# Optimization experiments

Hardware: AMD Instinct MI355X
Metric: run time of the kernel (lower is better)

Reference implementation:

```python
import jax, jax.numpy as jnp
import numpy as np

N_USER = 100000
N_ITEM = 100000
E = 500000
IN, HID, OUT = 128, 128, 64
ETYPES = ["rates", "rated_by", "follows", "similar"]
# canonical etypes: (user,rates,item), (item,rated_by,user), (user,follows,user), (item,similar,item)
SRC_N = {"rates": N_USER, "rated_by": N_ITEM, "follows": N_USER, "similar": N_ITEM}
DST_N = {"rates": N_ITEM, "rated_by": N_USER, "follows": N_USER, "similar": N_ITEM}


def setup_inputs() -> dict:
    key = jax.random.key(0)
    ks = iter(jax.random.split(key, 64))
    inp = {}
    inp["emb_user"] = jax.random.normal(next(ks), (N_USER, IN), jnp.float32)
    inp["emb_item"] = jax.random.normal(next(ks), (N_ITEM, IN), jnp.float32)
    for et in ETYPES:
        inp[f"W1_{et}"] = jax.random.normal(next(ks), (IN, HID), jnp.float32) / np.float32(np.sqrt(IN))
        inp[f"b1_{et}"] = jnp.zeros((HID,), jnp.float32)
        inp[f"W2_{et}"] = jax.random.normal(next(ks), (HID, OUT), jnp.float32) / np.float32(np.sqrt(HID))
        inp[f"b2_{et}"] = jnp.zeros((OUT,), jnp.float32)
    for et in ETYPES:
        inp[f"src_{et}"] = jax.random.randint(next(ks), (E,), 0, SRC_N[et], jnp.int32)
        inp[f"dst_{et}"] = jax.random.randint(next(ks), (E,), 0, DST_N[et], jnp.int32)
    return inp


def _mean_agg(Wh, src, dst, n_dst):
    """copy_u('Wh','m') + mean('m','h') for one relation."""
    m = jnp.take(Wh, src, axis=0)                                   # [E, d] gather
    s = jax.ops.segment_sum(m, dst, num_segments=n_dst)             # [n_dst, d]
    cnt = jax.ops.segment_sum(jnp.ones(src.shape, Wh.dtype), dst, num_segments=n_dst)
    return s / jnp.maximum(cnt, 1.0)[:, None]                       # zero-indegree -> 0


def _layer(xu, xi, Wr, br, Wrb, brb, Wf, bf, Ws, bs,
           s_r, d_r, s_rb, d_rb, s_f, d_f, s_s, d_s):
    # cross-etype 'sum' reducer
    h_user = (_mean_agg(xi @ Wrb + brb, s_rb, d_rb, N_USER)
              + _mean_agg(xu @ Wf + bf, s_f, d_f, N_USER))
    h_item = (_mean_agg(xu @ Wr + br, s_r, d_r, N_ITEM)
              + _mean_agg(xi @ Ws + bs, s_s, d_s, N_ITEM))
    return h_user, h_item


def reference(emb_user, emb_item,
              W1_rates, b1_rates, W1_rated_by, b1_rated_by, W1_follows, b1_follows, W1_similar, b1_similar,
              W2_rates, b2_rates, W2_rated_by, b2_rated_by, W2_follows, b2_follows, W2_similar, b2_similar,
              src_rates, dst_rates, src_rated_by, dst_rated_by,
              src_follows, dst_follows, src_similar, dst_similar):
    hu, hi = _layer(emb_user, emb_item,
                    W1_rates, b1_rates, W1_rated_by, b1_rated_by,
                    W1_follows, b1_follows, W1_similar, b1_similar,
                    src_rates, dst_rates, src_rated_by, dst_rated_by,
                    src_follows, dst_follows, src_similar, dst_similar)
    hu = jax.nn.leaky_relu(hu)  # torch F.leaky_relu default slope 0.01
    hi = jax.nn.leaky_relu(hi)
    ou, oi = _layer(hu, hi,
                    W2_rates, b2_rates, W2_rated_by, b2_rated_by,
                    W2_follows, b2_follows, W2_similar, b2_similar,
                    src_rates, dst_rates, src_rated_by, dst_rated_by,
                    src_follows, dst_follows, src_similar, dst_similar)
    return ou  # ret_obj == 'user'
```

## Files before the change

### kernel.cpp

```cpp
#include <hip/hip_runtime.h>
#include <hip/hip_fp16.h>

#define N_USER 100000
#define N_ITEM 100000
#define NEDGE  500000
#define NKEY   400000
#define BSHIFT 11
#define NB     196
#define BCAP   11264
#define TILE   4096

#define SEG_RATES    0
#define SEG_RATED_BY 100000
#define SEG_FOLLOWS  200000
#define SEG_SIMILAR  300000

typedef _Float16 f16x8 __attribute__((ext_vector_type(8)));
typedef float    f32x4 __attribute__((ext_vector_type(4)));

__global__ void prep_w_all(const float* __restrict__ W0, const float* __restrict__ W1,
                           const float* __restrict__ W2, const float* __restrict__ W3,
                           const float* __restrict__ W4, const float* __restrict__ W5,
                           __half* __restrict__ D0, __half* __restrict__ D1,
                           __half* __restrict__ D2, __half* __restrict__ D3,
                           __half* __restrict__ D4, __half* __restrict__ D5)
{
    int y = blockIdx.y;
    const float* W = y == 0 ? W0 : y == 1 ? W1 : y == 2 ? W2 : y == 3 ? W3 : y == 4 ? W4 : W5;
    __half* dst    = y == 0 ? D0 : y == 1 ? D1 : y == 2 ? D2 : y == 3 ? D3 : y == 4 ? D4 : D5;
    int N = y < 4 ? 128 : 64;
    int i = blockIdx.x * 256 + threadIdx.x;
    if (i >= 128 * N) return;
    int k = i / N, n = i % N;
    int chunk = (n >> 4) * 4 + (k >> 5);
    int lane  = ((k >> 3) & 3) * 16 + (n & 15);
    int e     = k & 7;
    dst[(chunk * 64 + lane) * 8 + e] = __float2half(W[i]);
}

__global__ __launch_bounds__(256, 3)
void gemm2(const float* __restrict__ A,
           const __half* __restrict__ Wf0, const __half* __restrict__ Wf1,
           const float* __restrict__ b0, const float* __restrict__ b1,
           __half* __restrict__ out0, __half* __restrict__ out1, int M)
{
    const int tid = threadIdx.x;
    const int wave = tid >> 6, lane = tid & 63;
    const int l16 = lane & 15, lk = lane >> 4;
    const int rowBase = blockIdx.x * 64 + wave * 16;

    f32x4 acc0[8], acc1[8];
#pragma unroll
    for (int n = 0; n < 8; ++n) { acc0[n] = (f32x4)0.f; acc1[n] = (f32x4)0.f; }

    const int gr = rowBase + l16;
    const bool valid = gr < M;
    const float* ap = A + (size_t)(valid ? gr : 0) * 128 + lk * 8;
    float4 av[8];
#pragma unroll
    for (int kt = 0; kt < 4; ++kt) {
        av[2 * kt]     = *reinterpret_cast<const float4*>(ap + kt * 32);
        av[2 * kt + 1] = *reinterpret_cast<const float4*>(ap + kt * 32 + 4);
    }
    if (!valid) {
#pragma unroll
        for (int j = 0; j < 8; ++j) av[j] = make_float4(0.f, 0.f, 0.f, 0.f);
    }

#pragma unroll
    for (int kt = 0; kt < 4; ++kt) {
        f16x8 af;
        af[0] = (_Float16)av[2 * kt].x;     af[1] = (_Float16)av[2 * kt].y;
        af[2] = (_Float16)av[2 * kt].z;     af[3] = (_Float16)av[2 * kt].w;
        af[4] = (_Float16)av[2 * kt + 1].x; af[5] = (_Float16)av[2 * kt + 1].y;
        af[6] = (_Float16)av[2 * kt + 1].z; af[7] = (_Float16)av[2 * kt + 1].w;
#pragma unroll
        for (int n = 0; n < 8; ++n) {
            const size_t cidx = (size_t)((n * 4 + kt) * 64 + lane) * 8;
            f16x8 bf0 = *reinterpret_cast<const f16x8*>(Wf0 + cidx);
            f16x8 bf1 = *reinterpret_cast<const f16x8*>(Wf1 + cidx);
            acc0[n] = __builtin_amdgcn_mfma_f32_16x16x32_f16(af, bf0, acc0[n], 0, 0, 0);
            acc1[n] = __builtin_amdgcn_mfma_f32_16x16x32_f16(af, bf1, acc1[n], 0, 0, 0);
        }
    }

    const int gr0 = rowBase + lk * 4;
#pragma unroll
    for (int n = 0; n < 8; ++n) {
        float bv0 = b0[n * 16 + l16];
        float bv1 = b1[n * 16 + l16];
#pragma unroll
        for (int r = 0; r < 4; ++r) {
            int grr = gr0 + r;
            if (grr < M) {
                out0[(size_t)grr * 128 + n * 16 + l16] = __float2half(acc0[n][r] + bv0);
                out1[(size_t)grr * 128 + n * 16 + l16] = __float2half(acc1[n][r] + bv1);
            }
        }
    }
}

__global__ __launch_bounds__(256, 4)
void gemm1_l2_pair(const __half* __restrict__ A0, const __half* __restrict__ A1,
                   const __half* __restrict__ Wf0, const __half* __restrict__ Wf1,
                   const float* __restrict__ bias0, const float* __restrict__ bias1,
                   __half* __restrict__ O0, __half* __restrict__ O1, int M)
{
    const __half* A  = blockIdx.y ? A1 : A0;
    const __half* Wf = blockIdx.y ? Wf1 : Wf0;
    const float* bias = blockIdx.y ? bias1 : bias0;
    __half* out = blockIdx.y ? O1 : O0;

    const int tid = threadIdx.x;
    const int wave = tid >> 6, lane = tid & 63;
    const int l16 = lane & 15, lk = lane >> 4;
    const int rowBase = blockIdx.x * 128 + wave * 32;

    f32x4 acc[2][4];
#pragma unroll
    for (int m = 0; m < 2; ++m)
#pragma unroll
        for (int n = 0; n < 4; ++n) acc[m][n] = (f32x4)0.f;

#pragma unroll
    for (int kt = 0; kt < 4; ++kt) {
        f16x8 af[2];
#pragma unroll
        for (int m = 0; m < 2; ++m) {
            int gr = rowBase + m * 16 + l16;
            f16x8 a = (f16x8)(_Float16)0.f;
            if (gr < M)
                a = *reinterpret_cast<const f16x8*>(&A[(size_t)gr * 128 + kt * 32 + lk * 8]);
#pragma unroll
            for (int e = 0; e < 8; ++e) {
                float x = (float)a[e];
                x = x > 0.f ? x : 0.01f * x;
                a[e] = (_Float16)x;
            }
            af[m] = a;
        }
#pragma unroll
        for (int n = 0; n < 4; ++n) {
            const size_t cidx = (size_t)((n * 4 + kt) * 64 + lane) * 8;
            f16x8 bf = *reinterpret_cast<const f16x8*>(Wf + cidx);
            acc[0][n] = __builtin_amdgcn_mfma_f32_16x16x32_f16(af[0], bf, acc[0][n], 0, 0, 0);
            acc[1][n] = __builtin_amdgcn_mfma_f32_16x16x32_f16(af[1], bf, acc[1][n], 0, 0, 0);
        }
    }

#pragma unroll
    for (int m = 0; m < 2; ++m) {
        int gr0 = rowBase + m * 16 + lk * 4;
#pragma unroll
        for (int n = 0; n < 4; ++n) {
            float bv = bias[n * 16 + l16];
#pragma unroll
            for (int r = 0; r < 4; ++r) {
                int gr = gr0 + r;
                if (gr < M)
                    out[(size_t)gr * 64 + n * 16 + l16] = __float2half(acc[m][n][r] + bv);
            }
        }
    }
}

__global__ __launch_bounds__(256)
void partition_kernel(const int* __restrict__ s0, const int* __restrict__ d0,
                      const int* __restrict__ s1, const int* __restrict__ d1,
                      const int* __restrict__ s2, const int* __restrict__ d2,
                      const int* __restrict__ s3, const int* __restrict__ d3,
                      int* __restrict__ bucket_cursor, uint2* __restrict__ pairbuf)
{
    __shared__ int cntS[256], lscan[256], gbase[256], cur[256];
    __shared__ uint2 stage[TILE];
    __shared__ unsigned char bslot[TILE];

    const int t = threadIdx.x;
    const int rel = blockIdx.y;
    const int* S = rel == 0 ? s0 : rel == 1 ? s1 : rel == 2 ? s2 : s3;
    const int* D = rel == 0 ? d0 : rel == 1 ? d1 : rel == 2 ? d2 : d3;
    const int tileBase = blockIdx.x * TILE;
    const int tileN = min(TILE, NEDGE - tileBase);

    cntS[t] = 0;
    __syncthreads();

    int key[16], sv[16];
#pragma unroll
    for (int k = 0; k < 16; ++k) {
        int i = tileBase + k * 256 + t;
        if (i < NEDGE) {
            sv[k]  = S[i];
            key[k] = rel * 100000 + D[i];
            atomicAdd(&cntS[key[k] >> BSHIFT], 1);
        } else key[k] = -1;
    }
    __syncthreads();

    const int c = cntS[t];
    lscan[t] = c;
    __syncthreads();
    for (int off = 1; off < 256; off <<= 1) {
        int v = (t >= off) ? lscan[t - off] : 0;
        __syncthreads();
        lscan[t] += v;
        __syncthreads();
    }
    const int ex = lscan[t] - c;
    __syncthreads();
    lscan[t] = ex;
    cur[t]   = ex;
    if (t < NB && c > 0) gbase[t] = atomicAdd(&bucket_cursor[t], c);
    __syncthreads();

#pragma unroll
    for (int k = 0; k < 16; ++k) {
        if (key[k] >= 0) {
            int b = key[k] >> BSHIFT;
            int slot = atomicAdd(&cur[b], 1);
            stage[slot] = make_uint2((unsigned)key[k], (unsigned)sv[k]);
            bslot[slot] = (unsigned char)b;
        }
    }
    __syncthreads();

    for (int j = t; j < tileN; j += 256) {
        int b = bslot[j];
        pairbuf[(size_t)b * BCAP + gbase[b] + (j - lscan[b])] = stage[j];
    }
}

__global__ __launch_bounds__(256)
void bucket_scan(const int* __restrict__ bucket_cursor, int* __restrict__ gstart,
                 int* __restrict__ row_start)
{
    __shared__ int sd[256];
    int t = threadIdx.x;
    int v = (t < NB) ? bucket_cursor[t] : 0;
    sd[t] = v;
    __syncthreads();
    for (int off = 1; off < 256; off <<= 1) {
        int u = (t >= off) ? sd[t - off] : 0;
        __syncthreads();
        sd[t] += u;
        __syncthreads();
    }
    if (t < NB) gstart[t] = sd[t] - v;
    if (t == NB) gstart[NB] = sd[NB - 1];
    if (t == 0)  row_start[NKEY] = 4 * NEDGE;
}

__global__ __launch_bounds__(256)
void build_csr(const uint2* __restrict__ pairbuf, const int* __restrict__ bucket_cursor,
               const int* __restrict__ gstart, int* __restrict__ row_start,
               int* __restrict__ csr_src)
{
    __shared__ int hist[2048];
    __shared__ int scan2[2048];
    __shared__ int partial[256];

    const int b = blockIdx.x;
    const int t = threadIdx.x;
    const int cnt = bucket_cursor[b];
    const int gs  = gstart[b];
    const uint2* pb = pairbuf + (size_t)b * BCAP;
    const int keyBase = b << BSHIFT;
    const int nbin = min(2048, NKEY - keyBase);

    for (int k = t; k < 2048; k += 256) hist[k] = 0;
    __syncthreads();
    for (int j = t; j < cnt; j += 256)
        atomicAdd(&hist[(int)pb[j].x - keyBase], 1);
    __syncthreads();

    const int base8 = t * 8;
    int s = 0;
#pragma unroll
    for (int k = 0; k < 8; ++k) s += hist[base8 + k];
    partial[t] = s;
    __syncthreads();
    for (int off = 1; off < 256; off <<= 1) {
        int u = (t >= off) ? partial[t - off] : 0;
        __syncthreads();
        partial[t] += u;
        __syncthreads();
    }
    int run = partial[t] - s;
#pragma unroll
    for (int k = 0; k < 8; ++k) { scan2[base8 + k] = run; run += hist[base8 + k]; }
    __syncthreads();

    for (int k = t; k < nbin; k += 256) row_start[keyBase + k] = gs + scan2[k];
    for (int k = t; k < 2048; k += 256) hist[k] = scan2[k];
    __syncthreads();

    for (int j = t; j < cnt; j += 256) {
        uint2 p = pb[j];
        int pos = atomicAdd(&hist[(int)p.x - keyBase], 1);
        csr_src[gs + pos] = (int)p.y;
    }
}

template<bool ACCUM>
__global__ __launch_bounds__(256)
void pull128_pair(const __half* __restrict__ WhA, int segA, __half* __restrict__ outA,
                  const __half* __restrict__ WhB, int segB, __half* __restrict__ outB,
                  const int* __restrict__ row_start, const int* __restrict__ csr_src)
{
    const __half* Wh = blockIdx.y ? WhB : WhA;
    __half* out      = blockIdx.y ? outB : outA;
    const int seg    = blockIdx.y ? segB : segA;

    const int wid = (blockIdx.x * 256 + threadIdx.x) >> 6;
    if (wid >= 100000) return;
    const int g  = (threadIdx.x >> 4) & 3;
    const int sl = threadIdx.x & 15;
    const int idx = seg + wid;
    const int s0 = row_start[idx], s1 = row_start[idx + 1];
    const float inv = 1.0f / (float)max(s1 - s0, 1);

    float acc[8];
#pragma unroll
    for (int j = 0; j < 8; ++j) acc[j] = 0.f;

    for (int e = s0 + g; e < s1; e += 4) {
        int src = csr_src[e];
        uint4 u = *reinterpret_cast<const uint4*>(&Wh[(size_t)src * 128 + sl * 8]);
        const __half2* hp = reinterpret_cast<const __half2*>(&u);
#pragma unroll
        for (int j = 0; j < 4; ++j) {
            float2 f = __half22float2(hp[j]);
            acc[2 * j] += f.x; acc[2 * j + 1] += f.y;
        }
    }
#pragma unroll
    for (int j = 0; j < 8; ++j) {
        acc[j] += __shfl_xor(acc[j], 16);
        acc[j] += __shfl_xor(acc[j], 32);
        acc[j] *= inv;
    }
    if (g == 0) {
        __half* o = out + (size_t)wid * 128 + sl * 8;
        if (ACCUM) {
            uint4 c = *reinterpret_cast<const uint4*>(o);
            const __half2* cp = reinterpret_cast<const __half2*>(&c);
#pragma unroll
            for (int j = 0; j < 4; ++j) {
                float2 f = __half22float2(cp[j]);
                acc[2 * j] += f.x; acc[2 * j + 1] += f.y;
            }
        }
        uint4 st;
        __half2* sp = reinterpret_cast<__half2*>(&st);
#pragma unroll
        for (int j = 0; j < 4; ++j) sp[j] = __floats2half2_rn(acc[2 * j], acc[2 * j + 1]);
        *reinterpret_cast<uint4*>(o) = st;
    }
}

__global__ __launch_bounds__(256)
void dual_pull64(const __half* __restrict__ WhRB, const __half* __restrict__ WhF,
                 const int* __restrict__ row_start, const int* __restrict__ csr_src,
                 float* __restrict__ out)
{
    const int wid = (blockIdx.x * 256 + threadIdx.x) >> 6;
    if (wid >= N_USER) return;
    const int g  = (threadIdx.x >> 4) & 3;
    const int sl = threadIdx.x & 15;

    const int rb0 = row_start[SEG_RATED_BY + wid], rb1 = row_start[SEG_RATED_BY + wid + 1];
    const int f0  = row_start[SEG_FOLLOWS  + wid], f1  = row_start[SEG_FOLLOWS  + wid + 1];
    const float invRB = 1.0f / (float)max(rb1 - rb0, 1);
    const float invF  = 1.0f / (float)max(f1 - f0, 1);

    const __half* Wh = (g < 2) ? WhRB : WhF;
    const int e0 = (g < 2) ? rb0 + (g & 1) : f0 + (g & 1);
    const int e1 = (g < 2) ? rb1 : f1;

    float acc[4] = {0.f, 0.f, 0.f, 0.f};
    for (int e = e0; e < e1; e += 2) {
        int src = csr_src[e];
        uint2 u = *reinterpret_cast<const uint2*>(&Wh[(size_t)src * 64 + sl * 4]);
        const __half2* hp = reinterpret_cast<const __half2*>(&u);
        float2 fa = __half22float2(hp[0]);
        float2 fb = __half22float2(hp[1]);
        acc[0] += fa.x; acc[1] += fa.y; acc[2] += fb.x; acc[3] += fb.y;
    }
    const float sc = (g < 2) ? invRB : invF;
#pragma unroll
    for (int j = 0; j < 4; ++j) {
        acc[j] += __shfl_xor(acc[j], 16);
        acc[j] *= sc;
        acc[j] += __shfl_xor(acc[j], 32);
    }
    if (g == 0) {
        float4 v = make_float4(acc[0], acc[1], acc[2], acc[3]);
        *reinterpret_cast<float4*>(&out[(size_t)wid * 64 + sl * 4]) = v;
    }
}

extern "C" void kernel_launch(void* const* d_in, const int* in_sizes, int n_in,
                              void* d_out, int out_size, void* d_ws, size_t ws_size,
                              hipStream_t stream)
{
    const float* emb_user = (const float*)d_in[0];
    const float* emb_item = (const float*)d_in[1];
    const float* W1_rates    = (const float*)d_in[2];
    const float* b1_rates    = (const float*)d_in[3];
    const float* W1_rated_by = (const float*)d_in[6];
    const float* b1_rated_by = (const float*)d_in[7];
    const float* W2_rated_by = (const float*)d_in[8];
    const float* b2_rated_by = (const float*)d_in[9];
    const float* W1_follows  = (const float*)d_in[10];
    const float* b1_follows  = (const float*)d_in[11];
    const float* W2_follows  = (const float*)d_in[12];
    const float* b2_follows  = (const float*)d_in[13];
    const float* W1_similar  = (const float*)d_in[14];
    const float* b1_similar  = (const float*)d_in[15];
    const int* src_rates    = (const int*)d_in[18];
    const int* dst_rates    = (const int*)d_in[19];
    const int* src_rated_by = (const int*)d_in[20];
    const int* dst_rated_by = (const int*)d_in[21];
    const int* src_follows  = (const int*)d_in[22];
    const int* dst_follows  = (const int*)d_in[23];
    const int* src_similar  = (const int*)d_in[24];
    const int* dst_similar  = (const int*)d_in[25];

    float* out = (float*)d_out;

    char* base = (char*)d_ws;
    __half* WhX  = (__half*)base;
    __half* WhY  = (__half*)(base + 25600000);
    __half* accI = (__half*)(base + 51200000);
    __half* accU = (__half*)(base + 76800000);
    int* csr_src   = (int*)(base + 102400000);
    int* row_start = (int*)(base + 110400000);
    int* bucket_cursor = (int*)(base + 112000016);
    int* gstart        = (int*)(base + 112001056);
    __half* wf = (__half*)(base + 112002080);
    __half* wf_rates    = wf;
    __half* wf_follows  = wf + 16384;
    __half* wf_similar  = wf + 32768;
    __half* wf_rated_by = wf + 49152;
    __half* wf2_rb      = wf + 65536;
    __half* wf2_f       = wf + 73728;
    uint2* pairbuf = (uint2*)WhX;

    hipMemsetAsync(bucket_cursor, 0, 256 * sizeof(int), stream);

    prep_w_all<<<dim3(64, 6), 256, 0, stream>>>(
        W1_rates, W1_follows, W1_similar, W1_rated_by, W2_rated_by, W2_follows,
        wf_rates, wf_follows, wf_similar, wf_rated_by, wf2_rb, wf2_f);

    const int tiles = (NEDGE + TILE - 1) / TILE;
    partition_kernel<<<dim3(tiles, 4), 256, 0, stream>>>(
        src_rates, dst_rates, src_rated_by, dst_rated_by,
        src_follows, dst_follows, src_similar, dst_similar,
        bucket_cursor, pairbuf);
    bucket_scan<<<1, 256, 0, stream>>>(bucket_cursor, gstart, row_start);
    build_csr<<<NB, 256, 0, stream>>>(pairbuf, bucket_cursor, gstart, row_start, csr_src);

    const int gb2 = (100000 + 63) / 64;
    const int gbl = (100000 + 127) / 128;
    const int pb  = (100000 + 3) / 4;

    gemm2<<<gb2, 256, 0, stream>>>(emb_user, wf_rates, wf_follows, b1_rates, b1_follows,
                                   WhX, WhY, N_USER);
    pull128_pair<false><<<dim3(pb, 2), 256, 0, stream>>>(
        WhX, SEG_RATES, accI, WhY, SEG_FOLLOWS, accU, row_start, csr_src);
    gemm2<<<gb2, 256, 0, stream>>>(emb_item, wf_similar, wf_rated_by, b1_similar, b1_rated_by,
                                   WhX, WhY, N_ITEM);
    pull128_pair<true><<<dim3(pb, 2), 256, 0, stream>>>(
        WhX, SEG_SIMILAR, accI, WhY, SEG_RATED_BY, accU, row_start, csr_src);

    gemm1_l2_pair<<<dim3(gbl, 2), 256, 0, stream>>>(
        accI, accU, wf2_rb, wf2_f, b2_rated_by, b2_follows, WhX, WhY, N_ITEM);
    dual_pull64<<<pb, 256, 0, stream>>>(WhX, WhY, row_start, csr_src, out);
}
```

Before: 331.6 us.

## Drop memset and scan launches, unroll gather loops by two

The bucket cursor memset moves into prep_w_all, and the separate bucket_scan launch goes away. Each build_csr block now computes its own bucket offset with a shared-memory reduction, so two launches and their gaps are removed. The pull128_pair and dual_pull64 edge-gather loops are unrolled by two, so two independent row loads are in flight per iteration. The cost is a redundant reduction in every build_csr block and slightly higher register use in the pull kernels.

```diff
diff --git a/kernel.cpp b/kernel.cpp
--- a/kernel.cpp
+++ b/kernel.cpp
@@ -23,9 +23,12 @@
                            const float* __restrict__ W4, const float* __restrict__ W5,
                            __half* __restrict__ D0, __half* __restrict__ D1,
                            __half* __restrict__ D2, __half* __restrict__ D3,
-                           __half* __restrict__ D4, __half* __restrict__ D5)
+                           __half* __restrict__ D4, __half* __restrict__ D5,
+                           int* __restrict__ bucket_cursor)
 {
     int y = blockIdx.y;
+    if (y == 0 && blockIdx.x == 0 && threadIdx.x < NB)
+        bucket_cursor[threadIdx.x] = 0;
     const float* W = y == 0 ? W0 : y == 1 ? W1 : y == 2 ? W2 : y == 3 ? W3 : y == 4 ? W4 : W5;
     __half* dst    = y == 0 ? D0 : y == 1 ? D1 : y == 2 ? D2 : y == 3 ? D3 : y == 4 ? D4 : D5;
     int N = y < 4 ? 128 : 64;
@@ -231,38 +234,25 @@
 }
 
 __global__ __launch_bounds__(256)
-void bucket_scan(const int* __restrict__ bucket_cursor, int* __restrict__ gstart,
-                 int* __restrict__ row_start)
-{
-    __shared__ int sd[256];
-    int t = threadIdx.x;
-    int v = (t < NB) ? bucket_cursor[t] : 0;
-    sd[t] = v;
-    __syncthreads();
-    for (int off = 1; off < 256; off <<= 1) {
-        int u = (t >= off) ? sd[t - off] : 0;
-        __syncthreads();
-        sd[t] += u;
-        __syncthreads();
-    }
-    if (t < NB) gstart[t] = sd[t] - v;
-    if (t == NB) gstart[NB] = sd[NB - 1];
-    if (t == 0)  row_start[NKEY] = 4 * NEDGE;
-}
-
-__global__ __launch_bounds__(256)
 void build_csr(const uint2* __restrict__ pairbuf, const int* __restrict__ bucket_cursor,
-               const int* __restrict__ gstart, int* __restrict__ row_start,
-               int* __restrict__ csr_src)
+               int* __restrict__ row_start, int* __restrict__ csr_src)
 {
     __shared__ int hist[2048];
     __shared__ int scan2[2048];
     __shared__ int partial[256];
+    __shared__ int red[256];
 
     const int b = blockIdx.x;
     const int t = threadIdx.x;
+
+    red[t] = (t < b) ? bucket_cursor[t] : 0;
+    __syncthreads();
+    for (int off = 128; off > 0; off >>= 1) {
+        if (t < off) red[t] += red[t + off];
+        __syncthreads();
+    }
+    const int gs = red[0];
     const int cnt = bucket_cursor[b];
-    const int gs  = gstart[b];
     const uint2* pb = pairbuf + (size_t)b * BCAP;
     const int keyBase = b << BSHIFT;
     const int nbin = min(2048, NKEY - keyBase);
@@ -292,6 +282,7 @@
 
     for (int k = t; k < nbin; k += 256) row_start[keyBase + k] = gs + scan2[k];
     for (int k = t; k < 2048; k += 256) hist[k] = scan2[k];
+    if (b == NB - 1 && t == 0) row_start[NKEY] = 4 * NEDGE;
     __syncthreads();
 
     for (int j = t; j < cnt; j += 256) {
@@ -323,14 +314,29 @@
 #pragma unroll
     for (int j = 0; j < 8; ++j) acc[j] = 0.f;
 
-    for (int e = s0 + g; e < s1; e += 4) {
-        int src = csr_src[e];
-        uint4 u = *reinterpret_cast<const uint4*>(&Wh[(size_t)src * 128 + sl * 8]);
-        const __half2* hp = reinterpret_cast<const __half2*>(&u);
+    int e = s0 + g;
+    for (; e + 4 < s1; e += 8) {
+        int i1 = csr_src[e];
+        int i2 = csr_src[e + 4];
+        uint4 u1 = *reinterpret_cast<const uint4*>(&Wh[(size_t)i1 * 128 + sl * 8]);
+        uint4 u2 = *reinterpret_cast<const uint4*>(&Wh[(size_t)i2 * 128 + sl * 8]);
+        const __half2* h1 = reinterpret_cast<const __half2*>(&u1);
+        const __half2* h2 = reinterpret_cast<const __half2*>(&u2);
 #pragma unroll
         for (int j = 0; j < 4; ++j) {
-            float2 f = __half22float2(hp[j]);
-            acc[2 * j] += f.x; acc[2 * j + 1] += f.y;
+            float2 f1 = __half22float2(h1[j]);
+            float2 f2 = __half22float2(h2[j]);
+            acc[2 * j] += f1.x + f2.x; acc[2 * j + 1] += f1.y + f2.y;
+        }
+    }
+    if (e < s1) {
+        int i1 = csr_src[e];
+        uint4 u1 = *reinterpret_cast<const uint4*>(&Wh[(size_t)i1 * 128 + sl * 8]);
+        const __half2* h1 = reinterpret_cast<const __half2*>(&u1);
+#pragma unroll
+        for (int j = 0; j < 4; ++j) {
+            float2 f1 = __half22float2(h1[j]);
+            acc[2 * j] += f1.x; acc[2 * j + 1] += f1.y;
         }
     }
 #pragma unroll
@@ -374,17 +380,28 @@
     const float invF  = 1.0f / (float)max(f1 - f0, 1);
 
     const __half* Wh = (g < 2) ? WhRB : WhF;
-    const int e0 = (g < 2) ? rb0 + (g & 1) : f0 + (g & 1);
+    int e       = (g < 2) ? rb0 + (g & 1) : f0 + (g & 1);
     const int e1 = (g < 2) ? rb1 : f1;
 
     float acc[4] = {0.f, 0.f, 0.f, 0.f};
-    for (int e = e0; e < e1; e += 2) {
-        int src = csr_src[e];
-        uint2 u = *reinterpret_cast<const uint2*>(&Wh[(size_t)src * 64 + sl * 4]);
-        const __half2* hp = reinterpret_cast<const __half2*>(&u);
-        float2 fa = __half22float2(hp[0]);
-        float2 fb = __half22float2(hp[1]);
-        acc[0] += fa.x; acc[1] += fa.y; acc[2] += fb.x; acc[3] += fb.y;
+    for (; e + 2 < e1; e += 4) {
+        int i1 = csr_src[e];
+        int i2 = csr_src[e + 2];
+        uint2 u1 = *reinterpret_cast<const uint2*>(&Wh[(size_t)i1 * 64 + sl * 4]);
+        uint2 u2 = *reinterpret_cast<const uint2*>(&Wh[(size_t)i2 * 64 + sl * 4]);
+        const __half2* h1 = reinterpret_cast<const __half2*>(&u1);
+        const __half2* h2 = reinterpret_cast<const __half2*>(&u2);
+        float2 a1 = __half22float2(h1[0]), b1v = __half22float2(h1[1]);
+        float2 a2 = __half22float2(h2[0]), b2v = __half22float2(h2[1]);
+        acc[0] += a1.x + a2.x; acc[1] += a1.y + a2.y;
+        acc[2] += b1v.x + b2v.x; acc[3] += b1v.y + b2v.y;
+    }
+    if (e < e1) {
+        int i1 = csr_src[e];
+        uint2 u1 = *reinterpret_cast<const uint2*>(&Wh[(size_t)i1 * 64 + sl * 4]);
+        const __half2* h1 = reinterpret_cast<const __half2*>(&u1);
+        float2 a1 = __half22float2(h1[0]), b1v = __half22float2(h1[1]);
+        acc[0] += a1.x; acc[1] += a1.y; acc[2] += b1v.x; acc[3] += b1v.y;
     }
     const float sc = (g < 2) ? invRB : invF;
 #pragma unroll
@@ -436,7 +453,6 @@
     int* csr_src   = (int*)(base + 102400000);
     int* row_start = (int*)(base + 110400000);
     int* bucket_cursor = (int*)(base + 112000016);
-    int* gstart        = (int*)(base + 112001056);
     __half* wf = (__half*)(base + 112002080);
     __half* wf_rates    = wf;
     __half* wf_follows  = wf + 16384;
@@ -446,19 +462,16 @@
     __half* wf2_f       = wf + 73728;
     uint2* pairbuf = (uint2*)WhX;
 
-    hipMemsetAsync(bucket_cursor, 0, 256 * sizeof(int), stream);
-
     prep_w_all<<<dim3(64, 6), 256, 0, stream>>>(
         W1_rates, W1_follows, W1_similar, W1_rated_by, W2_rated_by, W2_follows,
-        wf_rates, wf_follows, wf_similar, wf_rated_by, wf2_rb, wf2_f);
+        wf_rates, wf_follows, wf_similar, wf_rated_by, wf2_rb, wf2_f, bucket_cursor);
 
     const int tiles = (NEDGE + TILE - 1) / TILE;
     partition_kernel<<<dim3(tiles, 4), 256, 0, stream>>>(
         src_rates, dst_rates, src_rated_by, dst_rated_by,
         src_follows, dst_follows, src_similar, dst_similar,
         bucket_cursor, pairbuf);
-    bucket_scan<<<1, 256, 0, stream>>>(bucket_cursor, gstart, row_start);
-    build_csr<<<NB, 256, 0, stream>>>(pairbuf, bucket_cursor, gstart, row_start, csr_src);
+    build_csr<<<NB, 256, 0, stream>>>(pairbuf, bucket_cursor, row_start, csr_src);
 
     const int gb2 = (100000 + 63) / 64;
     const int gbl = (100000 + 127) / 128;
```

New measurement: 318.0 us. 4.1% less time.
